# Optimization experiments

Hardware: AMD Instinct MI355X
Metric: run time of the kernel (lower is better)

Reference implementation:

```python
import jax, jax.numpy as jnp
import numpy as np

H = 2048; NH = 8; NKV = 2; HD = 256; NREP = NH // NKV
DFF = 4096; PLD = 256; NLT = 35; NL = 8
WIN = 512; FULL = 4096; POS = 1000
EPS = 1e-6
PLE_PROJ_SCALE = H ** -0.5       # per_layer_model_projection_scale
PLE_IN_SCALE = 2.0 ** -0.5       # per_layer_input_scale
IS_FULL = [i % 5 == 4 for i in range(NL)]  # layer 4 is full attention


def _rms(x, w):
    return x * jax.lax.rsqrt(jnp.mean(x * x, axis=-1, keepdims=True) + EPS) * w


def _vnorm(x):
    return x * jax.lax.rsqrt(jnp.mean(x * x, axis=-1, keepdims=True) + EPS)


def _rot_half(x):
    a, b = jnp.split(x, 2, axis=-1)
    return jnp.concatenate([-b, a], axis=-1)


def _rope(x, cos, sin):
    return x * cos + _rot_half(x) * sin


def _gelu(x):
    return jax.nn.gelu(x, approximate=True)


def _forward(hidden_states, causal_mask_full, causal_mask_sliding, update_mask,
             per_layer_raw, cos_s, sin_s, cos_f, sin_f,
             K_sliding_in, V_sliding_in, K_full_in, V_full_in,
             Wq, Wk, Wv, Wo, q_norm_w, k_norm_w,
             ln_in_w, ln_post_attn_w, ln_pre_ff_w, ln_post_ff_w,
             Wgate, Wup, Wdown, W_pl_gate, W_pl_proj, ln_post_pl_w,
             layer_scalar, W_ple, ple_norm_w):
    # ---- per-layer embedding (PLE) combine (_compute_ple) ----
    proj = (hidden_states @ W_ple.T) * PLE_PROJ_SCALE           # (1,1,35*256)
    g = proj.reshape(1, NLT, PLD)
    # layer_norm([x,-x]) trick == RMSNorm over last dim
    g = g * jax.lax.rsqrt(jnp.mean(g * g, -1, keepdims=True) + EPS) * ple_norm_w
    plc = (g.reshape(1, 1, NLT * PLD) + per_layer_raw) * PLE_IN_SCALE

    hs = hidden_states
    Ks_out, Vs_out, Kf_out, Vf_out = [], [], [], []
    si = fi = 0
    scale = 1.0 / np.sqrt(HD).astype(np.float32)
    for i in range(NL):
        is_full = IS_FULL[i]
        cos, sin = (cos_f, sin_f) if is_full else (cos_s, sin_s)
        residual = hs
        h = _rms(hs, ln_in_w[i])                                # (1,1,H)
        q = (h @ Wq[i].T).reshape(1, 1, NH, HD).transpose(0, 2, 1, 3)   # (1,NH,1,HD)
        q = _rms(q, q_norm_w[i])
        q = _rope(q, cos, sin)
        k = (h @ Wk[i].T).reshape(1, 1, NKV, HD).transpose(0, 2, 1, 3)  # (1,NKV,1,HD)
        v = (h @ Wv[i].T).reshape(1, 1, NKV, HD).transpose(0, 2, 1, 3)
        k = _rms(k, k_norm_w[i])
        v = _vnorm(v)
        k = _rope(k, cos, sin)
        if is_full:
            Kn = K_full_in[fi][None] * (1.0 - update_mask) + k * update_mask
            Vn = V_full_in[fi][None] * (1.0 - update_mask) + v * update_mask
            Kf_out.append(Kn[0]); Vf_out.append(Vn[0]); fi += 1
            mask = causal_mask_full
        else:
            Kn = jnp.concatenate([K_sliding_in[si][None, :, 1:, :], k], axis=2)
            Vn = jnp.concatenate([V_sliding_in[si][None, :, 1:, :], v], axis=2)
            Ks_out.append(Kn[0]); Vs_out.append(Vn[0]); si += 1
            mask = causal_mask_sliding
        Ke = jnp.repeat(Kn, NREP, axis=1)                       # GQA expand (1,NH,L,HD)
        Ve = jnp.repeat(Vn, NREP, axis=1)
        scores = jnp.einsum('bhqd,bhkd->bhqk', q, Ke) * scale + mask
        attn = jnp.einsum('bhqk,bhkd->bhqd', jax.nn.softmax(scores, axis=-1), Ve)
        attn = attn.transpose(0, 2, 1, 3).reshape(1, 1, NH * HD)
        attn = attn @ Wo[i].T
        hs = residual + _rms(attn, ln_post_attn_w[i])
        # ---- GeGLU MLP ----
        residual = hs
        h2 = _rms(hs, ln_pre_ff_w[i])
        mlp = (_gelu(h2 @ Wgate[i].T) * (h2 @ Wup[i].T)) @ Wdown[i].T
        hs = residual + _rms(mlp, ln_post_ff_w[i])
        # ---- per-layer input gate ----
        residual = hs
        sl = plc[:, :, i * PLD:(i + 1) * PLD]                   # (1,1,PLD)
        gated = _gelu(hs @ W_pl_gate[i].T) * sl
        pl = gated @ W_pl_proj[i].T
        hs = residual + _rms(pl, ln_post_pl_w[i])
        hs = hs * layer_scalar[i]
    return (hs, jnp.stack(Ks_out), jnp.stack(Vs_out),
            jnp.stack(Kf_out), jnp.stack(Vf_out))


def setup_inputs() -> dict:
    key = jax.random.key(0)
    ks = jax.random.split(key, 26)
    n = lambda k, shape, s=0.02: jax.random.normal(k, shape, dtype=jnp.float32) * s
    w1 = lambda k, shape: 1.0 + n(k, shape)
    inv_freq = 1.0 / (10000.0 ** (jnp.arange(0, HD, 2, dtype=jnp.float32) / HD))
    ang = POS * inv_freq
    cos = jnp.concatenate([jnp.cos(ang), jnp.cos(ang)]).reshape(1, 1, 1, HD)
    sin = jnp.concatenate([jnp.sin(ang), jnp.sin(ang)]).reshape(1, 1, 1, HD)
    mask_full = jnp.where(jnp.arange(FULL) <= POS, 0.0, -1e9).astype(jnp.float32).reshape(1, 1, 1, FULL)
    mask_slide = jnp.zeros((1, 1, 1, WIN), jnp.float32)
    um = jnp.zeros((1, 1, FULL, 1), jnp.float32).at[0, 0, POS, 0].set(1.0)
    return {
        'hidden_states': n(ks[0], (1, 1, H), 1.0),
        'causal_mask_full': mask_full,
        'causal_mask_sliding': mask_slide,
        'update_mask': um,
        'per_layer_raw': n(ks[1], (1, 1, NLT * PLD), 1.0),
        'cos_s': cos, 'sin_s': sin, 'cos_f': cos, 'sin_f': sin,
        'K_sliding_in': n(ks[2], (7, NKV, WIN, HD), 1.0),
        'V_sliding_in': n(ks[3], (7, NKV, WIN, HD), 1.0),
        'K_full_in': n(ks[4], (1, NKV, FULL, HD), 1.0),
        'V_full_in': n(ks[5], (1, NKV, FULL, HD), 1.0),
        'Wq': n(ks[6], (NL, NH * HD, H)),
        'Wk': n(ks[7], (NL, NKV * HD, H)),
        'Wv': n(ks[8], (NL, NKV * HD, H)),
        'Wo': n(ks[9], (NL, H, NH * HD)),
        'q_norm_w': w1(ks[10], (NL, HD)),
        'k_norm_w': w1(ks[11], (NL, HD)),
        'ln_in_w': w1(ks[12], (NL, H)),
        'ln_post_attn_w': w1(ks[13], (NL, H)),
        'ln_pre_ff_w': w1(ks[14], (NL, H)),
        'ln_post_ff_w': w1(ks[15], (NL, H)),
        'Wgate': n(ks[16], (NL, DFF, H)),
        'Wup': n(ks[17], (NL, DFF, H)),
        'Wdown': n(ks[18], (NL, H, DFF)),
        'W_pl_gate': n(ks[19], (NL, PLD, H)),
        'W_pl_proj': n(ks[20], (NL, H, PLD)),
        'ln_post_pl_w': w1(ks[21], (NL, H)),
        'layer_scalar': jnp.ones((NL,), jnp.float32),
        'W_ple': n(ks[22], (NLT * PLD, H)),
        'ple_norm_w': w1(ks[23], (PLD,)),
    }


def reference(hidden_states, causal_mask_full, causal_mask_sliding, update_mask,
              per_layer_raw, cos_s, sin_s, cos_f, sin_f,
              K_sliding_in, V_sliding_in, K_full_in, V_full_in,
              Wq, Wk, Wv, Wo, q_norm_w, k_norm_w,
              ln_in_w, ln_post_attn_w, ln_pre_ff_w, ln_post_ff_w,
              Wgate, Wup, Wdown, W_pl_gate, W_pl_proj, ln_post_pl_w,
              layer_scalar, W_ple, ple_norm_w):
    return _forward(hidden_states, causal_mask_full, causal_mask_sliding, update_mask,
                    per_layer_raw, cos_s, sin_s, cos_f, sin_f,
                    K_sliding_in, V_sliding_in, K_full_in, V_full_in,
                    Wq, Wk, Wv, Wo, q_norm_w, k_norm_w,
                    ln_in_w, ln_post_attn_w, ln_pre_ff_w, ln_post_ff_w,
                    Wgate, Wup, Wdown, W_pl_gate, W_pl_proj, ln_post_pl_w,
                    layer_scalar, W_ple, ple_norm_w)
```

## Files before the change

kernel.cpp:

```cpp
#include <hip/hip_runtime.h>

#define H    2048
#define NH   8
#define NKV  2
#define HD   256
#define DFF  4096
#define PLD  256
#define NL   8
#define WIN  512
#define FULLS 4096
#define EPS  1e-6f
#define ATT_SCALE 0.0625f
#define PLE_PROJ_SCALE 0.022097086912079608f
#define PLE_IN_SCALE   0.7071067811865476f
#define MS   16
#define NB   512
#define NWAVE 2048
#define NGRP 32
#define GSZ  16
#define NSID 56

__device__ __forceinline__ float waveSum(float v) {
#pragma unroll
  for (int o = 32; o; o >>= 1) v += __shfl_xor(v, o);
  return v;
}
__device__ __forceinline__ float waveMax(float v) {
#pragma unroll
  for (int o = 32; o; o >>= 1) v = fmaxf(v, __shfl_xor(v, o));
  return v;
}
__device__ __forceinline__ float blockSum(float v) {
  __shared__ float red[4];
  int lane = threadIdx.x & 63, wid = threadIdx.x >> 6;
  v = waveSum(v);
  if (lane == 0) red[wid] = v;
  __syncthreads();
  float s = red[0] + red[1] + red[2] + red[3];
  __syncthreads();
  return s;
}
__device__ __forceinline__ float gelu_t(float x) {
  float x3 = x * x * x;
  return 0.5f * x * (1.f + tanhf(0.79788456080286536f * (x + 0.044715f * x3)));
}

__device__ __forceinline__ void ast(float* p, float v) {
  __hip_atomic_store(p, v, __ATOMIC_RELAXED, __HIP_MEMORY_SCOPE_AGENT);
}

__device__ __forceinline__ void gbar(int* cnt, int* top, int* go, int sid) {
  asm volatile("s_waitcnt vmcnt(0)" ::: "memory");
  __syncthreads();
  if (threadIdx.x == 0) {
    const int grp = blockIdx.x >> 4;
    int old = __hip_atomic_fetch_add(cnt + (sid * NGRP + grp) * 32, 1,
                                     __ATOMIC_RELAXED, __HIP_MEMORY_SCOPE_AGENT);
    if (old == GSZ - 1) {
      int o2 = __hip_atomic_fetch_add(top + sid * 32, 1,
                                      __ATOMIC_RELAXED, __HIP_MEMORY_SCOPE_AGENT);
      if (o2 == NGRP - 1) {
        for (int g = 0; g < NGRP; g++)
          __hip_atomic_store(go + g * 32, sid + 1, __ATOMIC_RELAXED,
                             __HIP_MEMORY_SCOPE_AGENT);
      }
    }
    while (__hip_atomic_load(go + grp * 32, __ATOMIC_RELAXED,
                             __HIP_MEMORY_SCOPE_AGENT) <= sid)
      __builtin_amdgcn_s_sleep(2);
  }
  __syncthreads();
}

__device__ __forceinline__ float dot4(float4 w, float4 x, float acc) {
  return fmaf(w.x, x.x, fmaf(w.y, x.y, fmaf(w.z, x.z, fmaf(w.w, x.w, acc))));
}

template <int C>
__device__ __forceinline__ float dotrow(const float* __restrict__ w,
                                        const float* __restrict__ x, int lane) {
  float acc = 0.f;
#pragma unroll
  for (int c = lane * 4; c < C; c += 256)
    acc = dot4(*(const float4*)(w + c), *(const float4*)(x + c), acc);
  return waveSum(acc);
}
template <int NPF>
__device__ __forceinline__ void prefetch_row(const float* __restrict__ w, int lane,
                                             float4* pre) {
#pragma unroll
  for (int k = 0; k < NPF; k++) pre[k] = *(const float4*)(w + lane * 4 + k * 256);
}
template <int NPF>
__device__ __forceinline__ float dot_pre(const float4* pre, const float* __restrict__ x,
                                         int lane) {
  float acc = 0.f;
#pragma unroll
  for (int k = 0; k < NPF; k++)
    acc = dot4(pre[k], *(const float4*)(x + lane * 4 + k * 256), acc);
  return acc;
}
template <int C, int OFS>
__device__ __forceinline__ float dot_rest(const float* __restrict__ w,
                                          const float* __restrict__ x, int lane,
                                          float acc) {
#pragma unroll
  for (int c = OFS + lane * 4; c < C; c += 256)
    acc = dot4(*(const float4*)(w + c), *(const float4*)(x + c), acc);
  return acc;
}

struct MegaP {
  const float *hidden, *mask_full, *um, *plr, *cos_s, *sin_s, *cos_f, *sin_f;
  const float *Ksl, *Vsl, *Kfu, *Vfu;
  const float *Wq, *Wk, *Wv, *Wo, *qnw, *knw, *lin, *lpa, *lpf, *lpff;
  const float *Wg, *Wu, *Wd, *Wpg, *Wpp, *lpl, *lsc, *Wple, *plw;
  float *out, *outKs, *outVs, *outKf, *outVf;
  float *projb, *qkvb, *attnb, *wob, *actb, *dnb, *gatedb, *plb;
  float *hs_new, *hs2, *hs3, *part_o, *part_ml;
  int *cnt, *top, *go, *acnt;
};

__global__ __launch_bounds__(256, 2) void k_mega(MegaP p) {
  const int t = threadIdx.x, lane = t & 63, wid = t >> 6, b = blockIdx.x;
  const int gw = b * 4 + wid;
  int sid = 0;

  __shared__ __align__(16) float xs[2048];
  __shared__ __align__(16) float s_kr[2][256], s_v[2][256], s_q[256], s_qt[256];
  __shared__ float s_sc[64], s_ml[2];
  __shared__ int s_last;

  float4 preB[8];
  bool hasB = false;

  for (int li = 0; li < NL; li++) {
    const bool isf = (li % 5 == 4);
    const float* cosp = isf ? p.cos_f : p.cos_s;
    const float* sinp = isf ? p.sin_f : p.sin_s;
    float* qkvL = p.qkvb + li * 3072;

    {
      float e[8];
      if (li == 0) {
#pragma unroll
        for (int k = 0; k < 8; k++) e[k] = p.hidden[t + 256 * k];
      } else {
        const float* pl  = p.plb + (li - 1) * 2048;
        const float* wpl = p.lpl + (size_t)(li - 1) * 2048;
        const float* hp  = p.hs3 + (li - 1) * 2048;
        float plv[8]; float ss = 0.f;
#pragma unroll
        for (int k = 0; k < 8; k++) { plv[k] = pl[t + 256 * k]; ss += plv[k] * plv[k]; }
        float r1 = rsqrtf(blockSum(ss) * (1.f / 2048.f) + EPS);
        float sc = p.lsc[li - 1];
#pragma unroll
        for (int k = 0; k < 8; k++) {
          int idx = t + 256 * k;
          e[k] = (hp[idx] + plv[k] * r1 * wpl[idx]) * sc;
        }
      }
      float ss2 = 0.f;
#pragma unroll
      for (int k = 0; k < 8; k++) ss2 += e[k] * e[k];
      float r2 = rsqrtf(blockSum(ss2) * (1.f / 2048.f) + EPS);
      const float* w_in = p.lin + (size_t)li * 2048;
      float* hsN = p.hs_new + li * 2048;
#pragma unroll
      for (int k = 0; k < 8; k++) {
        int idx = t + 256 * k;
        xs[idx] = e[k] * r2 * w_in[idx];
        if (b == 0) ast(hsN + idx, e[k]);
      }
      __syncthreads();
      const int nrows = (li == 0) ? 5120 : 3072;
      for (int row = gw; row < nrows; row += NWAVE) {
        const float* wr; const float* xsrc = xs; float* dst; float sc2 = 1.f;
        if (row < 2048)      { wr = p.Wq + ((size_t)li * 2048 + row) * H; dst = qkvL + row; }
        else if (row < 2560) { wr = p.Wk + ((size_t)li * 512 + (row - 2048)) * H; dst = qkvL + row; }
        else if (row < 3072) { wr = p.Wv + ((size_t)li * 512 + (row - 2560)) * H; dst = qkvL + row; }
        else { wr = p.Wple + (size_t)(row - 3072) * H; xsrc = p.hidden;
               dst = p.projb + (row - 3072); sc2 = PLE_PROJ_SCALE; }
        float s;
        if (row == gw && hasB) s = waveSum(dot_pre<8>(preB, xsrc, lane));
        else                   s = dotrow<2048>(wr, xsrc, lane);
        if (lane == 0) ast(dst, s * sc2);
      }
    }
    gbar(p.cnt, p.top, p.go, sid); sid++;

    {
      const int S = isf ? FULLS : WIN;
      const int nsp = isf ? 16 : 8;
      const int natt = NH * nsp;
      const int ncache = isf ? 256 : 32;
      const int ntask = natt + ncache;
      const int si = (li < 4) ? li : li - 1;
      const float* Kin = isf ? p.Kfu : p.Ksl + (size_t)si * 2 * WIN * HD;
      const float* Vin = isf ? p.Vfu : p.Vsl + (size_t)si * 2 * WIN * HD;
      float* Ko = isf ? p.outKf : p.outKs + (size_t)si * 2 * WIN * HD;
      float* Vo = isf ? p.outVf : p.outVs + (size_t)si * 2 * WIN * HD;
      float* pO  = p.part_o  + (size_t)li * (NH * MS * 256);
      float* pML = p.part_ml + li * (NH * MS * 2);

      if (b < ntask) {
        for (int c = 0; c < 2; c++) {
          float kvv = qkvL[2048 + c * 256 + t];
          float rk = rsqrtf(blockSum(kvv * kvv) * (1.f / 256.f) + EPS);
          float kn = kvv * rk * p.knw[li * 256 + t];
          s_qt[t] = kn;
          float vv = qkvL[2560 + c * 256 + t];
          float rv = rsqrtf(blockSum(vv * vv) * (1.f / 256.f) + EPS);
          float rot = (t < 128) ? -s_qt[t + 128] : s_qt[t - 128];
          s_kr[c][t] = kn * cosp[t] + rot * sinp[t];
          s_v[c][t] = vv * rv;
          __syncthreads();
        }
        const int task = b;
        if (task < natt) {
          const int h = task / nsp, split = task % nsp, kvh = h >> 2;
          const int j0 = split * 64;
          float qv = qkvL[h * 256 + t];
          float rq = rsqrtf(blockSum(qv * qv) * (1.f / 256.f) + EPS);
          float qn = qv * rq * p.qnw[li * 256 + t];
          s_qt[t] = qn;
          __syncthreads();
          float rot = (t < 128) ? -s_qt[t + 128] : s_qt[t - 128];
          s_q[t] = qn * cosp[t] + rot * sinp[t];
          __syncthreads();
          float4 q4 = ((const float4*)s_q)[lane];
          for (int jl = wid; jl < 64; jl += 4) {
            int j = j0 + jl;
            float4 k4;
            if (!isf) {
              k4 = (j < S - 1) ? ((const float4*)Kin)[((size_t)kvh * S + j + 1) * 64 + lane]
                               : ((const float4*)s_kr[kvh])[lane];
            } else {
              k4 = ((const float4*)Kin)[((size_t)kvh * S + j) * 64 + lane];
              float u = p.um[j];
              if (u != 0.f) {
                float om = 1.f - u;
                float4 nk = ((const float4*)s_kr[kvh])[lane];
                k4.x = k4.x * om + nk.x * u; k4.y = k4.y * om + nk.y * u;
                k4.z = k4.z * om + nk.z * u; k4.w = k4.w * om + nk.w * u;
              }
            }
            float pp = q4.x * k4.x + q4.y * k4.y + q4.z * k4.z + q4.w * k4.w;
            pp = waveSum(pp);
            if (lane == 0) s_sc[jl] = pp * ATT_SCALE + (isf ? p.mask_full[j] : 0.f);
          }
          __syncthreads();
          if (wid == 0) {
            float v = s_sc[lane];
            float m = waveMax(v);
            float e = expf(v - m);
            s_sc[lane] = e;
            float l = waveSum(e);
            if (lane == 0) { s_ml[0] = m; s_ml[1] = l; }
          }
          __syncthreads();
          float o = 0.f;
#pragma unroll 8
          for (int jl = 0; jl < 64; jl++) {
            int j = j0 + jl;
            float vj;
            if (!isf) {
              vj = (j < S - 1) ? Vin[((size_t)kvh * S + j + 1) * 256 + t] : s_v[kvh][t];
            } else {
              vj = Vin[((size_t)kvh * S + j) * 256 + t];
              float u = p.um[j];
              if (u != 0.f) vj = vj * (1.f - u) + s_v[kvh][t] * u;
            }
            o = fmaf(s_sc[jl], vj, o);
          }
          ast(pO + ((size_t)h * MS + split) * 256 + t, o);
          if (t < 2) ast(pML + (h * MS + split) * 2 + t, s_ml[t]);
          asm volatile("s_waitcnt vmcnt(0)" ::: "memory");
          __syncthreads();
          if (t == 0) {
            int old = __hip_atomic_fetch_add(p.acnt + li * NH + h, 1,
                                             __ATOMIC_RELAXED, __HIP_MEMORY_SCOPE_AGENT);
            s_last = (old == nsp - 1);
          }
          __syncthreads();
          if (s_last) {
            float M = -INFINITY;
            for (int s2 = 0; s2 < nsp; s2++) M = fmaxf(M, pML[(h * MS + s2) * 2]);
            float L = 0.f, oo = 0.f;
            for (int s2 = 0; s2 < nsp; s2++) {
              float m = pML[(h * MS + s2) * 2];
              float l = pML[(h * MS + s2) * 2 + 1];
              float f = expf(m - M);
              L += l * f;
              oo = fmaf(pO[((size_t)h * MS + s2) * 256 + t], f, oo);
            }
            ast(p.attnb + li * 2048 + h * 256 + t, oo / L);
          }
        } else {
          int ci = task - natt;
          const int fK = 2 * S * 64;
          const float4* Ki4 = (const float4*)Kin;
          const float4* Vi4 = (const float4*)Vin;
          float4* Ko4 = (float4*)Ko;
          float4* Vo4 = (float4*)Vo;
#pragma unroll
          for (int k = 0; k < 16; k++) {
            int idx = ci * 4096 + k * 256 + t;
            int isV = idx >= fK;
            int rid = isV ? idx - fK : idx;
            int kvh = rid / (S * 64);
            int rem = rid % (S * 64);
            int j = rem >> 6, d4 = rem & 63;
            const float4* in4 = isV ? Vi4 : Ki4;
            const float4* nn4 = (const float4*)(isV ? s_v[kvh] : s_kr[kvh]);
            float4 v;
            if (!isf) {
              v = (j < S - 1) ? in4[((size_t)kvh * S + j + 1) * 64 + d4] : nn4[d4];
            } else {
              v = in4[rid];
              float u = p.um[j];
              if (u != 0.f) {
                float om = 1.f - u;
                float4 nv = nn4[d4];
                v.x = v.x * om + nv.x * u; v.y = v.y * om + nv.y * u;
                v.z = v.z * om + nv.z * u; v.w = v.w * om + nv.w * u;
              }
            }
            (isV ? Vo4 : Ko4)[rid] = v;
          }
        }
      }
    }
    float4 preD[8];
    prefetch_row<8>(p.Wo + ((size_t)li * 2048 + gw) * H, lane, preD);
    gbar(p.cnt, p.top, p.go, sid); sid++;

    {
      float s = waveSum(dot_pre<8>(preD, p.attnb + li * 2048, lane));
      if (lane == 0) ast(p.wob + li * 2048 + gw, s);
    }
    float4 preG4[4], preU4[4];
    prefetch_row<4>(p.Wg + ((size_t)li * 4096 + gw) * H, lane, preG4);
    prefetch_row<4>(p.Wu + ((size_t)li * 4096 + gw) * H, lane, preU4);
    gbar(p.cnt, p.top, p.go, sid); sid++;

    {
      const float* hsN = p.hs_new + li * 2048;
      const float* wo = p.wob + li * 2048;
      const float* w_pa = p.lpa + (size_t)li * 2048;
      const float* w_pf = p.lpf + (size_t)li * 2048;
      float wv[8]; float ss = 0.f;
#pragma unroll
      for (int k = 0; k < 8; k++) { wv[k] = wo[t + 256 * k]; ss += wv[k] * wv[k]; }
      float r1 = rsqrtf(blockSum(ss) * (1.f / 2048.f) + EPS);
      float e[8]; float ss2 = 0.f;
#pragma unroll
      for (int k = 0; k < 8; k++) {
        int idx = t + 256 * k;
        e[k] = hsN[idx] + wv[k] * r1 * w_pa[idx];
        ss2 += e[k] * e[k];
      }
      float r2 = rsqrtf(blockSum(ss2) * (1.f / 2048.f) + EPS);
      float* hs2L = p.hs2 + li * 2048;
#pragma unroll
      for (int k = 0; k < 8; k++) {
        int idx = t + 256 * k;
        xs[idx] = e[k] * r2 * w_pf[idx];
        if (b == 0) ast(hs2L + idx, e[k]);
      }
      __syncthreads();
      {
        const float* g = p.Wg + ((size_t)li * 4096 + gw) * H;
        const float* u = p.Wu + ((size_t)li * 4096 + gw) * H;
        float ag = dot_rest<2048, 1024>(g, xs, lane, dot_pre<4>(preG4, xs, lane));
        float au = dot_rest<2048, 1024>(u, xs, lane, dot_pre<4>(preU4, xs, lane));
        ag = waveSum(ag); au = waveSum(au);
        if (lane == 0) ast(p.actb + li * 4096 + gw, gelu_t(ag) * au);
      }
      {
        int row = gw + 2048;
        const float* g = p.Wg + ((size_t)li * 4096 + row) * H;
        const float* u = p.Wu + ((size_t)li * 4096 + row) * H;
        float ag = 0.f, au = 0.f;
#pragma unroll
        for (int c = lane * 4; c < 2048; c += 256) {
          float4 x4 = *(const float4*)(xs + c);
          ag = dot4(*(const float4*)(g + c), x4, ag);
          au = dot4(*(const float4*)(u + c), x4, au);
        }
        ag = waveSum(ag); au = waveSum(au);
        if (lane == 0) ast(p.actb + li * 4096 + row, gelu_t(ag) * au);
      }
    }
    float4 preF[8];
    prefetch_row<8>(p.Wd + ((size_t)li * 2048 + gw) * DFF, lane, preF);
    gbar(p.cnt, p.top, p.go, sid); sid++;

    {
      const float* x = p.actb + li * 4096;
      const float* wr = p.Wd + ((size_t)li * 2048 + gw) * DFF;
      float s = waveSum(dot_rest<4096, 2048>(wr, x, lane, dot_pre<8>(preF, x, lane)));
      if (lane == 0) ast(p.dnb + li * 2048 + gw, s);
    }
    float4 preP[8];
    if (gw < 256) prefetch_row<8>(p.Wpg + ((size_t)li * 256 + gw) * H, lane, preP);
    gbar(p.cnt, p.top, p.go, sid); sid++;

    if (b < 64) {
      const float* hs2L = p.hs2 + li * 2048;
      const float* dn = p.dnb + li * 2048;
      const float* w_pff = p.lpff + (size_t)li * 2048;
      float dv[8]; float ss = 0.f;
#pragma unroll
      for (int k = 0; k < 8; k++) { dv[k] = dn[t + 256 * k]; ss += dv[k] * dv[k]; }
      float r1 = rsqrtf(blockSum(ss) * (1.f / 2048.f) + EPS);
      float* hs3L = p.hs3 + li * 2048;
#pragma unroll
      for (int k = 0; k < 8; k++) {
        int idx = t + 256 * k;
        float e = hs2L[idx] + dv[k] * r1 * w_pff[idx];
        xs[idx] = e;
        if (b == 0) ast(hs3L + idx, e);
      }
      float pv = p.projb[li * 256 + t];
      float rp = rsqrtf(blockSum(pv * pv) * (1.f / 256.f) + EPS);
      s_qt[t] = (pv * rp * p.plw[t] + p.plr[li * 256 + t]) * PLE_IN_SCALE;
      __syncthreads();
      float acc = waveSum(dot_pre<8>(preP, xs, lane));
      if (lane == 0) ast(p.gatedb + li * 256 + gw, gelu_t(acc) * s_qt[gw]);
    }
    float4 preH = *(const float4*)(p.Wpp + ((size_t)li * 2048 + gw) * PLD + lane * 4);
    gbar(p.cnt, p.top, p.go, sid); sid++;

    {
      float4 x4 = *(const float4*)(p.gatedb + li * 256 + lane * 4);
      float s = waveSum(dot4(preH, x4, 0.f));
      if (lane == 0) ast(p.plb + li * 2048 + gw, s);
    }
    hasB = (li + 1 < NL) && (gw < 3072);
    if (hasB) {
      const float* wr;
      if (gw < 2048)      wr = p.Wq + ((size_t)(li + 1) * 2048 + gw) * H;
      else if (gw < 2560) wr = p.Wk + ((size_t)(li + 1) * 512 + (gw - 2048)) * H;
      else                wr = p.Wv + ((size_t)(li + 1) * 512 + (gw - 2560)) * H;
      prefetch_row<8>(wr, lane, preB);
    }
    gbar(p.cnt, p.top, p.go, sid); sid++;
  }

  if (b == 0) {
    const float* pl = p.plb + 7 * 2048;
    const float* wpl = p.lpl + (size_t)7 * 2048;
    const float* hs3L = p.hs3 + 7 * 2048;
    float pv[8]; float ss = 0.f;
#pragma unroll
    for (int k = 0; k < 8; k++) { pv[k] = pl[t + 256 * k]; ss += pv[k] * pv[k]; }
    float r = rsqrtf(blockSum(ss) * (1.f / 2048.f) + EPS);
    float sc = p.lsc[NL - 1];
#pragma unroll
    for (int k = 0; k < 8; k++) {
      int idx = t + 256 * k;
      p.out[idx] = (hs3L[idx] + pv[k] * r * wpl[idx]) * sc;
    }
  }
}

extern "C" void kernel_launch(void* const* d_in, const int* in_sizes, int n_in,
                              void* d_out, int out_size, void* d_ws, size_t ws_size,
                              hipStream_t stream) {
  MegaP p;
  p.hidden     = (const float*)d_in[0];
  p.mask_full  = (const float*)d_in[1];
  p.um         = (const float*)d_in[3];
  p.plr        = (const float*)d_in[4];
  p.cos_s      = (const float*)d_in[5];
  p.sin_s      = (const float*)d_in[6];
  p.cos_f      = (const float*)d_in[7];
  p.sin_f      = (const float*)d_in[8];
  p.Ksl        = (const float*)d_in[9];
  p.Vsl        = (const float*)d_in[10];
  p.Kfu        = (const float*)d_in[11];
  p.Vfu        = (const float*)d_in[12];
  p.Wq         = (const float*)d_in[13];
  p.Wk         = (const float*)d_in[14];
  p.Wv         = (const float*)d_in[15];
  p.Wo         = (const float*)d_in[16];
  p.qnw        = (const float*)d_in[17];
  p.knw        = (const float*)d_in[18];
  p.lin        = (const float*)d_in[19];
  p.lpa        = (const float*)d_in[20];
  p.lpf        = (const float*)d_in[21];
  p.lpff       = (const float*)d_in[22];
  p.Wg         = (const float*)d_in[23];
  p.Wu         = (const float*)d_in[24];
  p.Wd         = (const float*)d_in[25];
  p.Wpg        = (const float*)d_in[26];
  p.Wpp        = (const float*)d_in[27];
  p.lpl        = (const float*)d_in[28];
  p.lsc        = (const float*)d_in[29];
  p.Wple       = (const float*)d_in[30];
  p.plw        = (const float*)d_in[31];

  float* out = (float*)d_out;
  const size_t KS_SZ = (size_t)7 * 2 * WIN * HD;
  const size_t KF_SZ = (size_t)2 * FULLS * HD;
  p.out   = out;
  p.outKs = out + 2048;
  p.outVs = p.outKs + KS_SZ;
  p.outKf = p.outVs + KS_SZ;
  p.outVf = p.outKf + KF_SZ;

  int* zi = (int*)d_ws;
  p.cnt  = zi;
  p.top  = zi + 57344;
  p.go   = zi + 57344 + 1792;
  p.acnt = zi + 57344 + 1792 + 1024;
  const size_t ZINTS = 57344 + 1792 + 1024 + 64;

  float* f = (float*)d_ws + ZINTS;
  p.projb  = f;  f += 2048;
  p.qkvb   = f;  f += NL * 3072;
  p.attnb  = f;  f += NL * 2048;
  p.wob    = f;  f += NL * 2048;
  p.actb   = f;  f += NL * 4096;
  p.dnb    = f;  f += NL * 2048;
  p.gatedb = f;  f += NL * 256;
  p.plb    = f;  f += NL * 2048;
  p.hs_new = f;  f += NL * 2048;
  p.hs2    = f;  f += NL * 2048;
  p.hs3    = f;  f += NL * 2048;
  p.part_o = f;  f += (size_t)NL * NH * MS * 256;
  p.part_ml= f;  f += NL * NH * MS * 2;

  (void)hipMemsetAsync(d_ws, 0, ZINTS * sizeof(int), stream);
  k_mega<<<NB, 256, 0, stream>>>(p);
}
```

Baseline: 677.9 us.

## Double grid to 1024 blocks and split Wo/Wdown rows across wave pairs

Doubles the persistent grid from 512 to 1024 blocks (occupancy hint raised to 4 blocks per CU) so each wave owns fewer weight rows. The Wo and Wdown matvecs are split into two half-row partial dots whose results are summed by the consumer, and the gate/up loop now covers all 4096 rows in a single pass. Grid-barrier waits use partial vmcnt so prefetches can stay in flight across the barrier, and the spin sleep is shortened. The cost is more barrier participants, doubled partial buffers, and tighter register budgets at 4 blocks per CU.

```diff
diff --git a/kernel.cpp b/kernel.cpp
--- a/kernel.cpp
+++ b/kernel.cpp
@@ -14,9 +14,9 @@
 #define PLE_PROJ_SCALE 0.022097086912079608f
 #define PLE_IN_SCALE   0.7071067811865476f
 #define MS   16
-#define NB   512
-#define NWAVE 2048
-#define NGRP 32
+#define NB   1024
+#define NWAVE 4096
+#define NGRP 64
 #define GSZ  16
 #define NSID 56
 
@@ -49,8 +49,44 @@
   __hip_atomic_store(p, v, __ATOMIC_RELAXED, __HIP_MEMORY_SCOPE_AGENT);
 }
 
-__device__ __forceinline__ void gbar(int* cnt, int* top, int* go, int sid) {
-  asm volatile("s_waitcnt vmcnt(0)" ::: "memory");
+__device__ __forceinline__ float dot4(float4 w, float4 x, float acc) {
+  return fmaf(w.x, x.x, fmaf(w.y, x.y, fmaf(w.z, x.z, fmaf(w.w, x.w, acc))));
+}
+template <int C>
+__device__ __forceinline__ float dotrow(const float* __restrict__ w,
+                                        const float* __restrict__ x, int lane) {
+  float acc = 0.f;
+#pragma unroll
+  for (int c = lane * 4; c < C; c += 256)
+    acc = dot4(*(const float4*)(w + c), *(const float4*)(x + c), acc);
+  return waveSum(acc);
+}
+template <int NPF>
+__device__ __forceinline__ void prefetch_row(const float* __restrict__ w, int lane,
+                                             float4* pre) {
+#pragma unroll
+  for (int k = 0; k < NPF; k++) pre[k] = *(const float4*)(w + lane * 4 + k * 256);
+}
+template <int NPF>
+__device__ __forceinline__ float dot_pre(const float4* pre, const float* __restrict__ x,
+                                         int lane) {
+  float acc = 0.f;
+#pragma unroll
+  for (int k = 0; k < NPF; k++)
+    acc = dot4(pre[k], *(const float4*)(x + k * 256 + lane * 4), acc);
+  return acc;
+}
+template <int C, int OFS>
+__device__ __forceinline__ float dot_rest(const float* __restrict__ w,
+                                          const float* __restrict__ x, int lane,
+                                          float acc) {
+#pragma unroll
+  for (int c = OFS + lane * 4; c < C; c += 256)
+    acc = dot4(*(const float4*)(w + c), *(const float4*)(x + c), acc);
+  return acc;
+}
+
+__device__ __forceinline__ void gbar_core(int* cnt, int* top, int* go, int sid) {
   __syncthreads();
   if (threadIdx.x == 0) {
     const int grp = blockIdx.x >> 4;
@@ -67,48 +103,15 @@
     }
     while (__hip_atomic_load(go + grp * 32, __ATOMIC_RELAXED,
                              __HIP_MEMORY_SCOPE_AGENT) <= sid)
-      __builtin_amdgcn_s_sleep(2);
+      __builtin_amdgcn_s_sleep(1);
   }
   __syncthreads();
 }
-
-__device__ __forceinline__ float dot4(float4 w, float4 x, float acc) {
-  return fmaf(w.x, x.x, fmaf(w.y, x.y, fmaf(w.z, x.z, fmaf(w.w, x.w, acc))));
-}
-
-template <int C>
-__device__ __forceinline__ float dotrow(const float* __restrict__ w,
-                                        const float* __restrict__ x, int lane) {
-  float acc = 0.f;
-#pragma unroll
-  for (int c = lane * 4; c < C; c += 256)
-    acc = dot4(*(const float4*)(w + c), *(const float4*)(x + c), acc);
-  return waveSum(acc);
-}
-template <int NPF>
-__device__ __forceinline__ void prefetch_row(const float* __restrict__ w, int lane,
-                                             float4* pre) {
-#pragma unroll
-  for (int k = 0; k < NPF; k++) pre[k] = *(const float4*)(w + lane * 4 + k * 256);
-}
-template <int NPF>
-__device__ __forceinline__ float dot_pre(const float4* pre, const float* __restrict__ x,
-                                         int lane) {
-  float acc = 0.f;
-#pragma unroll
-  for (int k = 0; k < NPF; k++)
-    acc = dot4(pre[k], *(const float4*)(x + lane * 4 + k * 256), acc);
-  return acc;
-}
-template <int C, int OFS>
-__device__ __forceinline__ float dot_rest(const float* __restrict__ w,
-                                          const float* __restrict__ x, int lane,
-                                          float acc) {
-#pragma unroll
-  for (int c = OFS + lane * 4; c < C; c += 256)
-    acc = dot4(*(const float4*)(w + c), *(const float4*)(x + c), acc);
-  return acc;
-}
+#define GBAR(NSTR) do { \
+  asm volatile("s_waitcnt vmcnt(" NSTR ")" ::: "memory"); \
+  gbar_core(p.cnt, p.top, p.go, sid); sid++; \
+} while (0)
+#define MEMPIN asm volatile("" ::: "memory")
 
 struct MegaP {
   const float *hidden, *mask_full, *um, *plr, *cos_s, *sin_s, *cos_f, *sin_f;
@@ -121,7 +124,7 @@
   int *cnt, *top, *go, *acnt;
 };
 
-__global__ __launch_bounds__(256, 2) void k_mega(MegaP p) {
+__global__ __launch_bounds__(256, 4) void k_mega(MegaP p) {
   const int t = threadIdx.x, lane = t & 63, wid = t >> 6, b = blockIdx.x;
   const int gw = b * 4 + wid;
   int sid = 0;
@@ -141,53 +144,57 @@
     float* qkvL = p.qkvb + li * 3072;
 
     {
-      float e[8];
-      if (li == 0) {
-#pragma unroll
-        for (int k = 0; k < 8; k++) e[k] = p.hidden[t + 256 * k];
-      } else {
-        const float* pl  = p.plb + (li - 1) * 2048;
-        const float* wpl = p.lpl + (size_t)(li - 1) * 2048;
-        const float* hp  = p.hs3 + (li - 1) * 2048;
-        float plv[8]; float ss = 0.f;
-#pragma unroll
-        for (int k = 0; k < 8; k++) { plv[k] = pl[t + 256 * k]; ss += plv[k] * plv[k]; }
-        float r1 = rsqrtf(blockSum(ss) * (1.f / 2048.f) + EPS);
-        float sc = p.lsc[li - 1];
+      const bool bActive = (li == 0) || (b < 768);
+      if (bActive) {
+        float e[8];
+        if (li == 0) {
+#pragma unroll
+          for (int k = 0; k < 8; k++) e[k] = p.hidden[t + 256 * k];
+        } else {
+          const float* pl  = p.plb + (li - 1) * 2048;
+          const float* wpl = p.lpl + (size_t)(li - 1) * 2048;
+          const float* hp  = p.hs3 + (li - 1) * 2048;
+          float plv[8]; float ss = 0.f;
+#pragma unroll
+          for (int k = 0; k < 8; k++) { plv[k] = pl[t + 256 * k]; ss += plv[k] * plv[k]; }
+          float r1 = rsqrtf(blockSum(ss) * (1.f / 2048.f) + EPS);
+          float sc = p.lsc[li - 1];
+#pragma unroll
+          for (int k = 0; k < 8; k++) {
+            int idx = t + 256 * k;
+            e[k] = (hp[idx] + plv[k] * r1 * wpl[idx]) * sc;
+          }
+        }
+        float ss2 = 0.f;
+#pragma unroll
+        for (int k = 0; k < 8; k++) ss2 += e[k] * e[k];
+        float r2 = rsqrtf(blockSum(ss2) * (1.f / 2048.f) + EPS);
+        const float* w_in = p.lin + (size_t)li * 2048;
+        float* hsN = p.hs_new + li * 2048;
 #pragma unroll
         for (int k = 0; k < 8; k++) {
           int idx = t + 256 * k;
-          e[k] = (hp[idx] + plv[k] * r1 * wpl[idx]) * sc;
+          xs[idx] = e[k] * r2 * w_in[idx];
+          if (b == 0) ast(hsN + idx, e[k]);
         }
-      }
-      float ss2 = 0.f;
-#pragma unroll
-      for (int k = 0; k < 8; k++) ss2 += e[k] * e[k];
-      float r2 = rsqrtf(blockSum(ss2) * (1.f / 2048.f) + EPS);
-      const float* w_in = p.lin + (size_t)li * 2048;
-      float* hsN = p.hs_new + li * 2048;
-#pragma unroll
-      for (int k = 0; k < 8; k++) {
-        int idx = t + 256 * k;
-        xs[idx] = e[k] * r2 * w_in[idx];
-        if (b == 0) ast(hsN + idx, e[k]);
-      }
-      __syncthreads();
-      const int nrows = (li == 0) ? 5120 : 3072;
-      for (int row = gw; row < nrows; row += NWAVE) {
-        const float* wr; const float* xsrc = xs; float* dst; float sc2 = 1.f;
-        if (row < 2048)      { wr = p.Wq + ((size_t)li * 2048 + row) * H; dst = qkvL + row; }
-        else if (row < 2560) { wr = p.Wk + ((size_t)li * 512 + (row - 2048)) * H; dst = qkvL + row; }
-        else if (row < 3072) { wr = p.Wv + ((size_t)li * 512 + (row - 2560)) * H; dst = qkvL + row; }
-        else { wr = p.Wple + (size_t)(row - 3072) * H; xsrc = p.hidden;
-               dst = p.projb + (row - 3072); sc2 = PLE_PROJ_SCALE; }
-        float s;
-        if (row == gw && hasB) s = waveSum(dot_pre<8>(preB, xsrc, lane));
-        else                   s = dotrow<2048>(wr, xsrc, lane);
-        if (lane == 0) ast(dst, s * sc2);
-      }
-    }
-    gbar(p.cnt, p.top, p.go, sid); sid++;
+        __syncthreads();
+        const int nrows = (li == 0) ? 5120 : 3072;
+        for (int row = gw; row < nrows; row += NWAVE) {
+          const float* wr; const float* xsrc = xs; float* dst; float sc2 = 1.f;
+          if (row < 2048)      { wr = p.Wq + ((size_t)li * 2048 + row) * H; dst = qkvL + row; }
+          else if (row < 2560) { wr = p.Wk + ((size_t)li * 512 + (row - 2048)) * H; dst = qkvL + row; }
+          else if (row < 3072) { wr = p.Wv + ((size_t)li * 512 + (row - 2560)) * H; dst = qkvL + row; }
+          else { wr = p.Wple + (size_t)(row - 3072) * H; xsrc = p.hidden;
+                 dst = p.projb + (row - 3072); sc2 = PLE_PROJ_SCALE; }
+          float s;
+          if (row == gw && hasB) s = waveSum(dot_pre<8>(preB, xsrc, lane));
+          else                   s = dotrow<2048>(wr, xsrc, lane);
+          if (lane == 0) ast(dst, s * sc2);
+        }
+      }
+    }
+    MEMPIN;
+    GBAR("0");
 
     {
       const int S = isf ? FULLS : WIN;
@@ -331,27 +338,35 @@
         }
       }
     }
-    float4 preD[8];
-    prefetch_row<8>(p.Wo + ((size_t)li * 2048 + gw) * H, lane, preD);
-    gbar(p.cnt, p.top, p.go, sid); sid++;
+    MEMPIN;
+    float4 preD[4];
+    prefetch_row<4>(p.Wo + ((size_t)li * 2048 + (gw >> 1)) * H + (gw & 1) * 1024,
+                    lane, preD);
+    GBAR("4");
 
     {
-      float s = waveSum(dot_pre<8>(preD, p.attnb + li * 2048, lane));
-      if (lane == 0) ast(p.wob + li * 2048 + gw, s);
-    }
+      int r = gw >> 1, half = gw & 1;
+      float s = waveSum(dot_pre<4>(preD, p.attnb + li * 2048 + half * 1024, lane));
+      if (lane == 0) ast(p.wob + li * 4096 + half * 2048 + r, s);
+    }
+    MEMPIN;
     float4 preG4[4], preU4[4];
     prefetch_row<4>(p.Wg + ((size_t)li * 4096 + gw) * H, lane, preG4);
     prefetch_row<4>(p.Wu + ((size_t)li * 4096 + gw) * H, lane, preU4);
-    gbar(p.cnt, p.top, p.go, sid); sid++;
+    GBAR("8");
 
     {
       const float* hsN = p.hs_new + li * 2048;
-      const float* wo = p.wob + li * 2048;
+      const float* wo = p.wob + li * 4096;
       const float* w_pa = p.lpa + (size_t)li * 2048;
       const float* w_pf = p.lpf + (size_t)li * 2048;
       float wv[8]; float ss = 0.f;
 #pragma unroll
-      for (int k = 0; k < 8; k++) { wv[k] = wo[t + 256 * k]; ss += wv[k] * wv[k]; }
+      for (int k = 0; k < 8; k++) {
+        int idx = t + 256 * k;
+        wv[k] = wo[idx] + wo[2048 + idx];
+        ss += wv[k] * wv[k];
+      }
       float r1 = rsqrtf(blockSum(ss) * (1.f / 2048.f) + EPS);
       float e[8]; float ss2 = 0.f;
 #pragma unroll
@@ -369,50 +384,39 @@
         if (b == 0) ast(hs2L + idx, e[k]);
       }
       __syncthreads();
-      {
-        const float* g = p.Wg + ((size_t)li * 4096 + gw) * H;
-        const float* u = p.Wu + ((size_t)li * 4096 + gw) * H;
-        float ag = dot_rest<2048, 1024>(g, xs, lane, dot_pre<4>(preG4, xs, lane));
-        float au = dot_rest<2048, 1024>(u, xs, lane, dot_pre<4>(preU4, xs, lane));
-        ag = waveSum(ag); au = waveSum(au);
-        if (lane == 0) ast(p.actb + li * 4096 + gw, gelu_t(ag) * au);
-      }
-      {
-        int row = gw + 2048;
-        const float* g = p.Wg + ((size_t)li * 4096 + row) * H;
-        const float* u = p.Wu + ((size_t)li * 4096 + row) * H;
-        float ag = 0.f, au = 0.f;
-#pragma unroll
-        for (int c = lane * 4; c < 2048; c += 256) {
-          float4 x4 = *(const float4*)(xs + c);
-          ag = dot4(*(const float4*)(g + c), x4, ag);
-          au = dot4(*(const float4*)(u + c), x4, au);
-        }
-        ag = waveSum(ag); au = waveSum(au);
-        if (lane == 0) ast(p.actb + li * 4096 + row, gelu_t(ag) * au);
-      }
-    }
+      const float* g = p.Wg + ((size_t)li * 4096 + gw) * H;
+      const float* u = p.Wu + ((size_t)li * 4096 + gw) * H;
+      float ag = waveSum(dot_rest<2048, 1024>(g, xs, lane, dot_pre<4>(preG4, xs, lane)));
+      float au = waveSum(dot_rest<2048, 1024>(u, xs, lane, dot_pre<4>(preU4, xs, lane)));
+      if (lane == 0) ast(p.actb + li * 4096 + gw, gelu_t(ag) * au);
+    }
+    MEMPIN;
     float4 preF[8];
-    prefetch_row<8>(p.Wd + ((size_t)li * 2048 + gw) * DFF, lane, preF);
-    gbar(p.cnt, p.top, p.go, sid); sid++;
+    prefetch_row<8>(p.Wd + ((size_t)li * 2048 + (gw >> 1)) * DFF + (gw & 1) * 2048,
+                    lane, preF);
+    GBAR("8");
 
     {
-      const float* x = p.actb + li * 4096;
-      const float* wr = p.Wd + ((size_t)li * 2048 + gw) * DFF;
-      float s = waveSum(dot_rest<4096, 2048>(wr, x, lane, dot_pre<8>(preF, x, lane)));
-      if (lane == 0) ast(p.dnb + li * 2048 + gw, s);
-    }
-    float4 preP[8];
-    if (gw < 256) prefetch_row<8>(p.Wpg + ((size_t)li * 256 + gw) * H, lane, preP);
-    gbar(p.cnt, p.top, p.go, sid); sid++;
-
+      int r = gw >> 1, half = gw & 1;
+      float s = waveSum(dot_pre<8>(preF, p.actb + li * 4096 + half * 2048, lane));
+      if (lane == 0) ast(p.dnb + li * 4096 + half * 2048 + r, s);
+    }
+    MEMPIN;
     if (b < 64) {
+      float4 preP[8];
+      prefetch_row<8>(p.Wpg + ((size_t)li * 256 + gw) * H, lane, preP);
+      GBAR("8");
+
       const float* hs2L = p.hs2 + li * 2048;
-      const float* dn = p.dnb + li * 2048;
+      const float* dn = p.dnb + li * 4096;
       const float* w_pff = p.lpff + (size_t)li * 2048;
       float dv[8]; float ss = 0.f;
 #pragma unroll
-      for (int k = 0; k < 8; k++) { dv[k] = dn[t + 256 * k]; ss += dv[k] * dv[k]; }
+      for (int k = 0; k < 8; k++) {
+        int idx = t + 256 * k;
+        dv[k] = dn[idx] + dn[2048 + idx];
+        ss += dv[k] * dv[k];
+      }
       float r1 = rsqrtf(blockSum(ss) * (1.f / 2048.f) + EPS);
       float* hs3L = p.hs3 + li * 2048;
 #pragma unroll
@@ -428,15 +432,21 @@
       __syncthreads();
       float acc = waveSum(dot_pre<8>(preP, xs, lane));
       if (lane == 0) ast(p.gatedb + li * 256 + gw, gelu_t(acc) * s_qt[gw]);
-    }
-    float4 preH = *(const float4*)(p.Wpp + ((size_t)li * 2048 + gw) * PLD + lane * 4);
-    gbar(p.cnt, p.top, p.go, sid); sid++;
-
-    {
+    } else {
+      GBAR("0");
+    }
+    MEMPIN;
+    float4 preH;
+    if (gw < 2048)
+      preH = *(const float4*)(p.Wpp + ((size_t)li * 2048 + gw) * PLD + lane * 4);
+    GBAR("1");
+
+    if (gw < 2048) {
       float4 x4 = *(const float4*)(p.gatedb + li * 256 + lane * 4);
       float s = waveSum(dot4(preH, x4, 0.f));
       if (lane == 0) ast(p.plb + li * 2048 + gw, s);
     }
+    MEMPIN;
     hasB = (li + 1 < NL) && (gw < 3072);
     if (hasB) {
       const float* wr;
@@ -445,7 +455,7 @@
       else                wr = p.Wv + ((size_t)(li + 1) * 512 + (gw - 2560)) * H;
       prefetch_row<8>(wr, lane, preB);
     }
-    gbar(p.cnt, p.top, p.go, sid); sid++;
+    GBAR("8");
   }
 
   if (b == 0) {
@@ -512,18 +522,18 @@
 
   int* zi = (int*)d_ws;
   p.cnt  = zi;
-  p.top  = zi + 57344;
-  p.go   = zi + 57344 + 1792;
-  p.acnt = zi + 57344 + 1792 + 1024;
-  const size_t ZINTS = 57344 + 1792 + 1024 + 64;
+  p.top  = zi + 114688;
+  p.go   = zi + 114688 + 1792;
+  p.acnt = zi + 114688 + 1792 + 2048;
+  const size_t ZINTS = 114688 + 1792 + 2048 + 64;
 
   float* f = (float*)d_ws + ZINTS;
   p.projb  = f;  f += 2048;
   p.qkvb   = f;  f += NL * 3072;
   p.attnb  = f;  f += NL * 2048;
-  p.wob    = f;  f += NL * 2048;
+  p.wob    = f;  f += NL * 4096;
   p.actb   = f;  f += NL * 4096;
-  p.dnb    = f;  f += NL * 2048;
+  p.dnb    = f;  f += NL * 4096;
   p.gatedb = f;  f += NL * 256;
   p.plb    = f;  f += NL * 2048;
   p.hs_new = f;  f += NL * 2048;
```

New measurement: 823.1 us. +21.4%, slower.
